# Kernel tuning notes

Measured on AMD Instinct MI355X. Metric: run time of the kernel, lower is better.

## Reference

```python
import jax, jax.numpy as jnp
import numpy as np

IOU_THR = 0.5      # global_nms default
SCORE_THR = 0.5    # global_nms default
SCORE_BONUS = 0.05 # _match_queries_to_prompt_boxes combined score bonus


def _box_iou_matrix(a, b):
    # a: [P,4], b: [Q,4] in xyxy
    lt = jnp.maximum(a[:, None, :2], b[None, :, :2])
    rb = jnp.minimum(a[:, None, 2:], b[None, :, 2:])
    wh = jnp.clip(rb - lt, 0.0)
    inter = wh[..., 0] * wh[..., 1]
    area_a = jnp.clip(a[:, 2] - a[:, 0], 0.0) * jnp.clip(a[:, 3] - a[:, 1], 0.0)
    area_b = jnp.clip(b[:, 2] - b[:, 0], 0.0) * jnp.clip(b[:, 3] - b[:, 1], 0.0)
    union = area_a[:, None] + area_b[None, :] - inter
    return jnp.where(union > 0.0, inter / union, 0.0)


def _rand_boxes(key, n, size):
    pts = jax.random.uniform(key, (n, 2, 2)) * size
    lt = jnp.min(pts, axis=1)
    rb = jnp.max(pts, axis=1)
    return jnp.concatenate([lt, rb], axis=-1)


def setup_inputs() -> dict:
    key = jax.random.key(0)
    k1, k2, k3, k4 = jax.random.split(key, 4)
    N, H, W, P = 96, 512, 512, 8
    mask_logits = jax.random.normal(k1, (N, H, W), dtype=jnp.float32)
    scores = jax.random.uniform(k2, (N,), dtype=jnp.float32)
    prompt_boxes = _rand_boxes(k3, P, float(W)).astype(jnp.float32)
    query_boxes = _rand_boxes(k4, N, float(W)).astype(jnp.float32)
    return {"mask_logits": mask_logits, "scores": scores,
            "prompt_boxes": prompt_boxes, "query_boxes": query_boxes}


def reference(mask_logits, scores, prompt_boxes, query_boxes):
    N = mask_logits.shape[0]
    # ---- pairwise mask IoU (batched, replaces per-pair mask_iou + .item syncs) ----
    m = (mask_logits > 0.0).astype(mask_logits.dtype).reshape(N, -1)  # [N,HW]
    inter = m @ m.T                                                    # [N,N]
    area = m.sum(-1)
    union = area[:, None] + area[None, :] - inter
    iou = jnp.where(union > 0.0, inter / union, 0.0)

    # ---- greedy mask NMS (global_nms) ----
    eligible = scores >= SCORE_THR
    eligible = jnp.where(jnp.any(eligible), eligible, jnp.ones_like(eligible))
    order = jnp.argsort(-scores)            # descending score, like pairs.sort
    iou_s = iou[order][:, order]
    elig_s = eligible[order]

    def nms_step(kept, i):
        sup = jnp.any(kept & (iou_s[i] > IOU_THR))
        k_i = elig_s[i] & (~sup)
        return kept.at[i].set(k_i), None

    kept_s, _ = jax.lax.scan(nms_step, jnp.zeros((N,), bool), jnp.arange(N))
    keep = jnp.zeros((N,), bool).at[order].set(kept_s)
    nms_scores = scores * keep.astype(scores.dtype)   # [N]

    # ---- greedy box-to-query bipartite matching ----
    bi = _box_iou_matrix(prompt_boxes, query_boxes)   # [P,Q]
    combined = bi + SCORE_BONUS * scores[None, :]
    P, Q = combined.shape
    flat_order = jnp.argsort(-combined.reshape(-1))   # candidates, best first
    ps = flat_order // Q
    qs = flat_order % Q

    def match_step(state, pq):
        assigned, used, assign = state
        p, q = pq
        take = (~assigned[p]) & (~used[q])
        assigned = assigned.at[p].set(assigned[p] | take)
        used = used.at[q].set(used[q] | take)
        assign = assign.at[p].set(jnp.where(take, q, assign[p]))
        return (assigned, used, assign), None

    init = (jnp.zeros((P,), bool), jnp.zeros((Q,), bool),
            jnp.full((P,), -1, dtype=jnp.int32))
    (assigned, used, assign), _ = jax.lax.scan(match_step, init,
                                               (ps.astype(jnp.int32), qs.astype(jnp.int32)))

    # fallback: unmatched prompts take highest-score unused query
    def fb_step(state, p):
        used, assign = state
        need = assign[p] < 0
        q = jnp.argmax(jnp.where(used, -jnp.inf, scores)).astype(jnp.int32)
        assign = assign.at[p].set(jnp.where(need, q, assign[p]))
        used = used.at[q].set(used[q] | need)
        return (used, assign), None

    (used, assign), _ = jax.lax.scan(fb_step, (used, assign), jnp.arange(P))
    matched_combined = combined[jnp.arange(P), assign]  # [P]

    return jnp.concatenate([nms_scores, matched_combined])
```

## Files before the change

kernel.cpp:

```cpp
#include <hip/hip_runtime.h>
#include <cstdint>
#include <cstddef>

#define N_MASKS 96
#define HW (512 * 512)
#define WORDS_PER_ROW (HW / 64)
#define TOTAL_WORDS (N_MASKS * WORDS_PER_ROW)
#define P_BOXES 8
#define IOU_THR 0.5f
#define SCORE_THR 0.5f
#define SCORE_BONUS 0.05f
#define TILE 4

__global__ __launch_bounds__(256) void pack_kernel(
    const float4* __restrict__ logits,
    unsigned long long* __restrict__ bits) {
  int wave = (blockIdx.x * blockDim.x + threadIdx.x) >> 6;
  int lane = threadIdx.x & 63;
  size_t g0 = (size_t)wave * 4;
  float4 v0 = logits[(g0 + 0) * 64 + lane];
  float4 v1 = logits[(g0 + 1) * 64 + lane];
  float4 v2 = logits[(g0 + 2) * 64 + lane];
  float4 v3 = logits[(g0 + 3) * 64 + lane];
  unsigned long long m[16];
  m[0]  = __ballot(v0.x > 0.0f); m[1]  = __ballot(v0.y > 0.0f);
  m[2]  = __ballot(v0.z > 0.0f); m[3]  = __ballot(v0.w > 0.0f);
  m[4]  = __ballot(v1.x > 0.0f); m[5]  = __ballot(v1.y > 0.0f);
  m[6]  = __ballot(v1.z > 0.0f); m[7]  = __ballot(v1.w > 0.0f);
  m[8]  = __ballot(v2.x > 0.0f); m[9]  = __ballot(v2.y > 0.0f);
  m[10] = __ballot(v2.z > 0.0f); m[11] = __ballot(v2.w > 0.0f);
  m[12] = __ballot(v3.x > 0.0f); m[13] = __ballot(v3.y > 0.0f);
  m[14] = __ballot(v3.z > 0.0f); m[15] = __ballot(v3.w > 0.0f);
  if (lane == 0) {
    unsigned long long* dst = bits + g0 * 4;
#pragma unroll
    for (int k = 0; k < 16; ++k) dst[k] = m[k];
  }
}

__global__ __launch_bounds__(256) void inter_kernel(
    const unsigned long long* __restrict__ bits,
    int* __restrict__ inter) {
  int bi = blockIdx.y * TILE, bj = blockIdx.x * TILE;
  if (bj + TILE - 1 < bi) return;
  int t = threadIdx.x;
  const ulonglong2* base = (const ulonglong2*)bits;
  int acc[TILE * TILE];
#pragma unroll
  for (int k = 0; k < TILE * TILE; ++k) acc[k] = 0;

#pragma unroll
  for (int w = 0; w < (WORDS_PER_ROW / 2) / 256; ++w) {
    int idx = w * 256 + t;
    ulonglong2 a[TILE], b[TILE];
#pragma unroll
    for (int r = 0; r < TILE; ++r)
      a[r] = base[(size_t)(bi + r) * (WORDS_PER_ROW / 2) + idx];
#pragma unroll
    for (int c = 0; c < TILE; ++c)
      b[c] = base[(size_t)(bj + c) * (WORDS_PER_ROW / 2) + idx];
#pragma unroll
    for (int r = 0; r < TILE; ++r)
#pragma unroll
      for (int c = 0; c < TILE; ++c)
        acc[r * TILE + c] += __popcll(a[r].x & b[c].x) + __popcll(a[r].y & b[c].y);
  }
#pragma unroll
  for (int k = 0; k < TILE * TILE; ++k)
    for (int off = 32; off >= 1; off >>= 1) acc[k] += __shfl_xor(acc[k], off);
  __shared__ int red[4][TILE * TILE];
  int wv = t >> 6;
  if ((t & 63) == 0) {
#pragma unroll
    for (int k = 0; k < TILE * TILE; ++k) red[wv][k] = acc[k];
  }
  __syncthreads();
  if (t < TILE * TILE) {
    int tot = red[0][t] + red[1][t] + red[2][t] + red[3][t];
    int i = bi + (t >> 2), j = bj + (t & 3);
    if (j >= i) {
      inter[i * N_MASKS + j] = tot;
      inter[j * N_MASKS + i] = tot;
    }
  }
}

__global__ __launch_bounds__(128) void finalize_kernel(
    const int* __restrict__ inter,
    const float* __restrict__ scores,
    const float* __restrict__ pboxes,
    const float* __restrict__ qboxes,
    float* __restrict__ out) {
  __shared__ float s_scores[N_MASKS];
  __shared__ float s_iou[N_MASKS * N_MASKS];
  __shared__ int s_order[N_MASKS];
  __shared__ float s_comb[P_BOXES * N_MASKS];
  __shared__ float s_pb[P_BOXES * 4];
  __shared__ float s_qb[N_MASKS * 4];
  int t = threadIdx.x;

  if (t < N_MASKS) s_scores[t] = scores[t];
  for (int k = t; k < P_BOXES * 4; k += 128) s_pb[k] = pboxes[k];
  for (int k = t; k < N_MASKS * 4; k += 128) s_qb[k] = qboxes[k];
  __syncthreads();

  for (int e = t; e < N_MASKS * N_MASKS; e += 128) {
    int i = e / N_MASKS, j = e % N_MASKS;
    float in_ = (float)inter[e];
    float un = (float)inter[i * N_MASKS + i] + (float)inter[j * N_MASKS + j] - in_;
    s_iou[e] = (un > 0.0f) ? in_ / un : 0.0f;
  }
  if (t < N_MASKS) {
    float sc = s_scores[t];
    int r = 0;
    for (int m = 0; m < N_MASKS; ++m) {
      float sm = s_scores[m];
      if (sm > sc || (sm == sc && m < t)) ++r;
    }
    s_order[r] = t;
  }
  for (int f = t; f < P_BOXES * N_MASKS; f += 128) {
    int p = f / N_MASKS, q = f % N_MASKS;
    float ax0 = s_pb[p * 4 + 0], ay0 = s_pb[p * 4 + 1];
    float ax1 = s_pb[p * 4 + 2], ay1 = s_pb[p * 4 + 3];
    float bx0 = s_qb[q * 4 + 0], by0 = s_qb[q * 4 + 1];
    float bx1 = s_qb[q * 4 + 2], by1 = s_qb[q * 4 + 3];
    float ltx = fmaxf(ax0, bx0), lty = fmaxf(ay0, by0);
    float rbx = fminf(ax1, bx1), rby = fminf(ay1, by1);
    float w = fmaxf(rbx - ltx, 0.0f), h = fmaxf(rby - lty, 0.0f);
    float in_ = w * h;
    float aa = fmaxf(ax1 - ax0, 0.0f) * fmaxf(ay1 - ay0, 0.0f);
    float ab = fmaxf(bx1 - bx0, 0.0f) * fmaxf(by1 - by0, 0.0f);
    float un = aa + ab - in_;
    float iou = (un > 0.0f) ? in_ / un : 0.0f;
    s_comb[f] = iou + SCORE_BONUS * s_scores[q];
  }
  __syncthreads();

  int lane = t & 63;
  if (t < 64) {
    bool e1 = (lane < N_MASKS) && (s_scores[lane] >= SCORE_THR);
    bool e2 = (lane + 64 < N_MASKS) && (s_scores[lane + 64] >= SCORE_THR);
    bool any_elig = __any(e1 || e2);
    unsigned long long kept_lo = 0, kept_hi = 0;
    for (int i = 0; i < N_MASKS; ++i) {
      int oi = s_order[i];
      bool c = false;
      if (lane < i && ((kept_lo >> lane) & 1ull))
        c = s_iou[oi * N_MASKS + s_order[lane]] > IOU_THR;
      int j2 = lane + 64;
      if (j2 < i && ((kept_hi >> lane) & 1ull))
        c |= s_iou[oi * N_MASKS + s_order[j2]] > IOU_THR;
      bool sup = __any(c);
      bool elig = any_elig ? (s_scores[oi] >= SCORE_THR) : true;
      if (elig && !sup) {
        if (i < 64) kept_lo |= 1ull << i;
        else kept_hi |= 1ull << (i - 64);
      }
    }
    for (int i = lane; i < N_MASKS; i += 64) {
      int oi = s_order[i];
      bool k = (i < 64) ? ((kept_lo >> i) & 1ull) : ((kept_hi >> (i - 64)) & 1ull);
      out[oi] = k ? s_scores[oi] : 0.0f;
    }
  } else {
    unsigned assigned_p = 0;
    unsigned long long used_lo = 0, used_hi = 0;
    int assign_q[P_BOXES];
#pragma unroll
    for (int p = 0; p < P_BOXES; ++p) assign_q[p] = -1;

    for (int it = 0; it < P_BOXES; ++it) {
      float bv = -1.0f;
      int bf = 1 << 30;
#pragma unroll
      for (int k = 0; k < (P_BOXES * N_MASKS) / 64; ++k) {
        int f = lane + 64 * k;
        int p = f / N_MASKS, q = f % N_MASKS;
        bool pv = !((assigned_p >> p) & 1u);
        bool qv = (q < 64) ? !((used_lo >> q) & 1ull) : !((used_hi >> (q - 64)) & 1ull);
        if (pv && qv) {
          float v = s_comb[f];
          if (v > bv || (v == bv && f < bf)) { bv = v; bf = f; }
        }
      }
      for (int off = 32; off >= 1; off >>= 1) {
        float ov = __shfl_xor(bv, off);
        int of = __shfl_xor(bf, off);
        if (ov > bv || (ov == bv && of < bf)) { bv = ov; bf = of; }
      }
      if (bf < (1 << 30)) {
        int p = bf / N_MASKS, q = bf % N_MASKS;
        assigned_p |= 1u << p;
        if (q < 64) used_lo |= 1ull << q;
        else used_hi |= 1ull << (q - 64);
        assign_q[p] = q;
      }
    }
#pragma unroll
    for (int p = 0; p < P_BOXES; ++p) {
      if (assign_q[p] < 0) {
        float best = -1e30f;
        int bq = 0;
        for (int q = 0; q < N_MASKS; ++q) {
          bool used = (q < 64) ? ((used_lo >> q) & 1ull) : ((used_hi >> (q - 64)) & 1ull);
          float v = used ? -1e30f : s_scores[q];
          if (v > best) { best = v; bq = q; }
        }
        assign_q[p] = bq;
        if (bq < 64) used_lo |= 1ull << bq;
        else used_hi |= 1ull << (bq - 64);
      }
    }
#pragma unroll
    for (int p = 0; p < P_BOXES; ++p) {
      if (lane == p) out[N_MASKS + p] = s_comb[p * N_MASKS + assign_q[p]];
    }
  }
}

extern "C" void kernel_launch(void* const* d_in, const int* in_sizes, int n_in,
                              void* d_out, int out_size, void* d_ws, size_t ws_size,
                              hipStream_t stream) {
  const float* mask_logits = (const float*)d_in[0];
  const float* scores = (const float*)d_in[1];
  const float* pboxes = (const float*)d_in[2];
  const float* qboxes = (const float*)d_in[3];
  float* out = (float*)d_out;

  unsigned long long* bits = (unsigned long long*)d_ws;
  int* inter = (int*)((char*)d_ws + (size_t)TOTAL_WORDS * sizeof(unsigned long long));

  int total_waves = (TOTAL_WORDS / 4) / 4;
  int pack_blocks = (total_waves * 64) / 256;
  pack_kernel<<<pack_blocks, 256, 0, stream>>>((const float4*)mask_logits, bits);

  dim3 g2(N_MASKS / TILE, N_MASKS / TILE);
  inter_kernel<<<g2, 256, 0, stream>>>(bits, inter);

  finalize_kernel<<<1, 128, 0, stream>>>(inter, scores, pboxes, qboxes, out);
}
```

Before: 65.92 us.

## Fuse intersection and finalize kernels via last-block ticket, compact tile grid

```diff
diff --git a/kernel.cpp b/kernel.cpp
--- a/kernel.cpp
+++ b/kernel.cpp
@@ -5,16 +5,20 @@
 #define N_MASKS 96
 #define HW (512 * 512)
 #define WORDS_PER_ROW (HW / 64)
+#define VECS_PER_ROW (WORDS_PER_ROW / 2)
 #define TOTAL_WORDS (N_MASKS * WORDS_PER_ROW)
 #define P_BOXES 8
-#define IOU_THR 0.5f
 #define SCORE_THR 0.5f
 #define SCORE_BONUS 0.05f
 #define TILE 4
+#define NT (N_MASKS / TILE)
+#define ACTIVE_TILES (NT * (NT + 1) / 2)
 
 __global__ __launch_bounds__(256) void pack_kernel(
     const float4* __restrict__ logits,
-    unsigned long long* __restrict__ bits) {
+    unsigned long long* __restrict__ bits,
+    int* counter) {
+  if (blockIdx.x == 0 && threadIdx.x == 0) *counter = 0;
   int wave = (blockIdx.x * blockDim.x + threadIdx.x) >> 6;
   int lane = threadIdx.x & 63;
   size_t g0 = (size_t)wave * 4;
@@ -38,37 +42,52 @@
   }
 }
 
-__global__ __launch_bounds__(256) void inter_kernel(
+__global__ __launch_bounds__(256) void inter_finalize_kernel(
     const unsigned long long* __restrict__ bits,
-    int* __restrict__ inter) {
-  int bi = blockIdx.y * TILE, bj = blockIdx.x * TILE;
-  if (bj + TILE - 1 < bi) return;
+    int* inter, int* counter,
+    const float* __restrict__ scores,
+    const float* __restrict__ pboxes,
+    const float* __restrict__ qboxes,
+    float* __restrict__ out) {
+  __shared__ int red[4][TILE * TILE];
+  __shared__ bool s_last;
+  __shared__ int s_int[N_MASKS * N_MASKS];
+  __shared__ float s_scores[N_MASKS];
+  __shared__ int s_order[N_MASKS];
+  __shared__ float s_comb[P_BOXES * N_MASKS];
+  __shared__ float s_pb[P_BOXES * 4];
+  __shared__ float s_qb[N_MASKS * 4];
+
   int t = threadIdx.x;
+
+  int b = blockIdx.x, ty = 0;
+  while (b >= NT - ty) { b -= NT - ty; ++ty; }
+  int tx = ty + b;
+  int bi = ty * TILE, bj = tx * TILE;
+
   const ulonglong2* base = (const ulonglong2*)bits;
   int acc[TILE * TILE];
 #pragma unroll
   for (int k = 0; k < TILE * TILE; ++k) acc[k] = 0;
-
-#pragma unroll
-  for (int w = 0; w < (WORDS_PER_ROW / 2) / 256; ++w) {
+#pragma unroll
+  for (int w = 0; w < VECS_PER_ROW / 256; ++w) {
     int idx = w * 256 + t;
-    ulonglong2 a[TILE], b[TILE];
+    ulonglong2 a[TILE], bb[TILE];
 #pragma unroll
     for (int r = 0; r < TILE; ++r)
-      a[r] = base[(size_t)(bi + r) * (WORDS_PER_ROW / 2) + idx];
+      a[r] = base[(size_t)(bi + r) * VECS_PER_ROW + idx];
 #pragma unroll
     for (int c = 0; c < TILE; ++c)
-      b[c] = base[(size_t)(bj + c) * (WORDS_PER_ROW / 2) + idx];
+      bb[c] = base[(size_t)(bj + c) * VECS_PER_ROW + idx];
 #pragma unroll
     for (int r = 0; r < TILE; ++r)
 #pragma unroll
       for (int c = 0; c < TILE; ++c)
-        acc[r * TILE + c] += __popcll(a[r].x & b[c].x) + __popcll(a[r].y & b[c].y);
+        acc[r * TILE + c] += __popcll(a[r].x & bb[c].x) + __popcll(a[r].y & bb[c].y);
   }
 #pragma unroll
   for (int k = 0; k < TILE * TILE; ++k)
     for (int off = 32; off >= 1; off >>= 1) acc[k] += __shfl_xor(acc[k], off);
-  __shared__ int red[4][TILE * TILE];
   int wv = t >> 6;
   if ((t & 63) == 0) {
 #pragma unroll
@@ -79,37 +98,25 @@
     int tot = red[0][t] + red[1][t] + red[2][t] + red[3][t];
     int i = bi + (t >> 2), j = bj + (t & 3);
     if (j >= i) {
-      inter[i * N_MASKS + j] = tot;
-      inter[j * N_MASKS + i] = tot;
-    }
-  }
-}
-
-__global__ __launch_bounds__(128) void finalize_kernel(
-    const int* __restrict__ inter,
-    const float* __restrict__ scores,
-    const float* __restrict__ pboxes,
-    const float* __restrict__ qboxes,
-    float* __restrict__ out) {
-  __shared__ float s_scores[N_MASKS];
-  __shared__ float s_iou[N_MASKS * N_MASKS];
-  __shared__ int s_order[N_MASKS];
-  __shared__ float s_comb[P_BOXES * N_MASKS];
-  __shared__ float s_pb[P_BOXES * 4];
-  __shared__ float s_qb[N_MASKS * 4];
-  int t = threadIdx.x;
+      __hip_atomic_store(&inter[i * N_MASKS + j], tot, __ATOMIC_RELAXED, __HIP_MEMORY_SCOPE_AGENT);
+      __hip_atomic_store(&inter[j * N_MASKS + i], tot, __ATOMIC_RELAXED, __HIP_MEMORY_SCOPE_AGENT);
+    }
+  }
+  __syncthreads();
+  if (t == 0) {
+    int ticket = __hip_atomic_fetch_add(counter, 1, __ATOMIC_ACQ_REL, __HIP_MEMORY_SCOPE_AGENT);
+    s_last = (ticket == ACTIVE_TILES - 1);
+  }
+  __syncthreads();
+  if (!s_last) return;
 
   if (t < N_MASKS) s_scores[t] = scores[t];
-  for (int k = t; k < P_BOXES * 4; k += 128) s_pb[k] = pboxes[k];
-  for (int k = t; k < N_MASKS * 4; k += 128) s_qb[k] = qboxes[k];
-  __syncthreads();
-
-  for (int e = t; e < N_MASKS * N_MASKS; e += 128) {
-    int i = e / N_MASKS, j = e % N_MASKS;
-    float in_ = (float)inter[e];
-    float un = (float)inter[i * N_MASKS + i] + (float)inter[j * N_MASKS + j] - in_;
-    s_iou[e] = (un > 0.0f) ? in_ / un : 0.0f;
-  }
+  for (int k = t; k < P_BOXES * 4; k += 256) s_pb[k] = pboxes[k];
+  for (int k = t; k < N_MASKS * 4; k += 256) s_qb[k] = qboxes[k];
+  for (int e = t; e < N_MASKS * N_MASKS; e += 256)
+    s_int[e] = __hip_atomic_load(&inter[e], __ATOMIC_RELAXED, __HIP_MEMORY_SCOPE_AGENT);
+  __syncthreads();
+
   if (t < N_MASKS) {
     float sc = s_scores[t];
     int r = 0;
@@ -119,7 +126,7 @@
     }
     s_order[r] = t;
   }
-  for (int f = t; f < P_BOXES * N_MASKS; f += 128) {
+  for (int f = t; f < P_BOXES * N_MASKS; f += 256) {
     int p = f / N_MASKS, q = f % N_MASKS;
     float ax0 = s_pb[p * 4 + 0], ay0 = s_pb[p * 4 + 1];
     float ax1 = s_pb[p * 4 + 2], ay1 = s_pb[p * 4 + 3];
@@ -137,33 +144,48 @@
   }
   __syncthreads();
 
-  int lane = t & 63;
   if (t < 64) {
-    bool e1 = (lane < N_MASKS) && (s_scores[lane] >= SCORE_THR);
-    bool e2 = (lane + 64 < N_MASKS) && (s_scores[lane + 64] >= SCORE_THR);
-    bool any_elig = __any(e1 || e2);
-    unsigned long long kept_lo = 0, kept_hi = 0;
+    int lane = t;
+    int oc1 = s_order[lane];
+    int oc2 = (lane < 32) ? s_order[lane + 64] : 0;
+    int a1 = s_int[oc1 * N_MASKS + oc1];
+    int a2 = s_int[oc2 * N_MASKS + oc2];
+    unsigned long long c1_lo = 0, c1_hi = 0, c2_lo = 0, c2_hi = 0;
     for (int i = 0; i < N_MASKS; ++i) {
       int oi = s_order[i];
-      bool c = false;
-      if (lane < i && ((kept_lo >> lane) & 1ull))
-        c = s_iou[oi * N_MASKS + s_order[lane]] > IOU_THR;
-      int j2 = lane + 64;
-      if (j2 < i && ((kept_hi >> lane) & 1ull))
-        c |= s_iou[oi * N_MASKS + s_order[j2]] > IOU_THR;
+      int ai = s_int[oi * N_MASKS + oi];
+      bool t1 = 3 * s_int[oi * N_MASKS + oc1] > ai + a1;
+      bool t2 = (lane < 32) && (3 * s_int[oi * N_MASKS + oc2] > ai + a2);
+      unsigned long long bit = 1ull << (i & 63);
+      if (i < 64) { if (t1) c1_lo |= bit; if (t2) c2_lo |= bit; }
+      else        { if (t1) c1_hi |= bit; if (t2) c2_hi |= bit; }
+    }
+    unsigned long long el_lo = __ballot(s_scores[oc1] >= SCORE_THR);
+    unsigned long long el_hi = __ballot((lane < 32) && (s_scores[oc2] >= SCORE_THR));
+    if ((el_lo | el_hi) == 0ull) { el_lo = ~0ull; el_hi = ~0ull; }
+
+    bool k1 = false, k2 = false;
+    for (int i = 0; i < N_MASKS; ++i) {
+      bool c;
+      bool el;
+      if (i < 64) {
+        unsigned long long bit = 1ull << i;
+        c = (k1 && (c1_lo & bit)) || (k2 && (c2_lo & bit));
+        el = (el_lo >> i) & 1ull;
+      } else {
+        unsigned long long bit = 1ull << (i - 64);
+        c = (k1 && (c1_hi & bit)) || (k2 && (c2_hi & bit));
+        el = (el_hi >> (i - 64)) & 1ull;
+      }
       bool sup = __any(c);
-      bool elig = any_elig ? (s_scores[oi] >= SCORE_THR) : true;
-      if (elig && !sup) {
-        if (i < 64) kept_lo |= 1ull << i;
-        else kept_hi |= 1ull << (i - 64);
-      }
-    }
-    for (int i = lane; i < N_MASKS; i += 64) {
-      int oi = s_order[i];
-      bool k = (i < 64) ? ((kept_lo >> i) & 1ull) : ((kept_hi >> (i - 64)) & 1ull);
-      out[oi] = k ? s_scores[oi] : 0.0f;
-    }
-  } else {
+      bool ki = el && !sup;
+      if (lane == i) k1 = ki;
+      if (lane + 64 == i) k2 = ki;
+    }
+    out[oc1] = k1 ? s_scores[oc1] : 0.0f;
+    if (lane < 32) out[oc2] = k2 ? s_scores[oc2] : 0.0f;
+  } else if (t < 128) {
+    int lane = t & 63;
     unsigned assigned_p = 0;
     unsigned long long used_lo = 0, used_hi = 0;
     int assign_q[P_BOXES];
@@ -230,13 +252,12 @@
 
   unsigned long long* bits = (unsigned long long*)d_ws;
   int* inter = (int*)((char*)d_ws + (size_t)TOTAL_WORDS * sizeof(unsigned long long));
+  int* counter = inter + N_MASKS * N_MASKS;
 
   int total_waves = (TOTAL_WORDS / 4) / 4;
   int pack_blocks = (total_waves * 64) / 256;
-  pack_kernel<<<pack_blocks, 256, 0, stream>>>((const float4*)mask_logits, bits);
-
-  dim3 g2(N_MASKS / TILE, N_MASKS / TILE);
-  inter_kernel<<<g2, 256, 0, stream>>>(bits, inter);
-
-  finalize_kernel<<<1, 128, 0, stream>>>(inter, scores, pboxes, qboxes, out);
+  pack_kernel<<<pack_blocks, 256, 0, stream>>>((const float4*)mask_logits, bits, counter);
+
+  inter_finalize_kernel<<<ACTIVE_TILES, 256, 0, stream>>>(
+      bits, inter, counter, scores, pboxes, qboxes, out);
 }
```

Measured after the change: 70.25 us. 1.07x slower.
